# Kernel tuning notes

Hardware: AMD Instinct MI355X
Metric: run time of the kernel (lower is better)

Reference implementation:

```python
import jax, jax.numpy as jnp
import numpy as np

B, S, HIDDEN = 8, 2048, 1024
NUM_GROUPS, NUM_VARS = 2, 320
CODEVECTOR_DIM = 256
TAU = 2.0  # module hardcodes self.temperature = 2
EPS_U = 1e-6


def setup_inputs() -> dict:
    key = jax.random.key(0)
    k1, k2, k3, k4 = jax.random.split(key, 4)
    hidden_states = jax.random.normal(k1, (B, S, HIDDEN), dtype=jnp.float32)
    W = jax.random.normal(k2, (NUM_GROUPS * NUM_VARS, HIDDEN), dtype=jnp.float32) * 0.02
    b = jnp.zeros((NUM_GROUPS * NUM_VARS,), dtype=jnp.float32)
    codevectors = jax.random.normal(
        k3, (1, NUM_GROUPS * NUM_VARS, CODEVECTOR_DIM // NUM_GROUPS), dtype=jnp.float32)
    gumbel_u = jax.random.uniform(
        k4, (B * S * NUM_GROUPS, NUM_VARS), minval=EPS_U, maxval=1.0 - EPS_U, dtype=jnp.float32)
    return {"hidden_states": hidden_states, "W": W, "b": b,
            "codevectors": codevectors, "gumbel_u": gumbel_u}


def reference(hidden_states, W, b, codevectors, gumbel_u):
    Bs, Ss, H = hidden_states.shape
    G, V = NUM_GROUPS, NUM_VARS
    N = Bs * Ss
    # weight_proj: [B,S,H] -> [B,S,G*V]
    logits = jnp.einsum('bsh,vh->bsv', hidden_states, W) + b
    logits = logits.reshape(N * G, V)
    # gumbel_softmax(tau=2, hard=True) -- training path
    gumbel = -jnp.log(-jnp.log(gumbel_u))
    y_soft = jax.nn.softmax((logits + gumbel) / TAU, axis=-1)
    idx = jnp.argmax(y_soft, axis=-1)
    y_hard = jax.nn.one_hot(idx, V, dtype=y_soft.dtype)
    # straight-through (hard value, soft gradient)
    codevector_probs = y_hard + y_soft - jax.lax.stop_gradient(y_soft)
    # perplexity over the soft (non-gumbel) distribution
    soft_dist = jax.nn.softmax(logits.reshape(N, G, V), axis=-1)
    marginal = soft_dist.mean(axis=0)                      # [G, V]
    perplexity = jnp.exp(-jnp.sum(marginal * jnp.log(marginal + 1e-7), axis=-1)).sum()
    # one-hot probs x codevectors, grouped sum: [N,G,V] x [G,V,d] -> [N,G,d]
    cv = codevectors.reshape(G, V, CODEVECTOR_DIM // G)
    out = jnp.einsum('ngv,gvd->ngd', codevector_probs.reshape(N, G, V), cv)
    out = out.reshape(Bs, Ss, CODEVECTOR_DIM)
    return out, perplexity
```

## Files before the change

### kernel.cpp

```cpp
#include <hip/hip_runtime.h>
#include <math.h>

#define NROWS 16384
#define HIDDEN 1024
#define NVARS 320
#define NCOLS 640
#define CVDIM 256
#define OUT_ELEMS (NROWS * CVDIM)

#define BM 64
#define BK 32
#define NTHREADS 512
#define LGS 324
#define BUFS 12288

typedef __attribute__((ext_vector_type(8))) short short8;
typedef __attribute__((ext_vector_type(4))) float floatx4;

__device__ __forceinline__ unsigned f32_to_bf16(float f) {
    unsigned u = __builtin_bit_cast(unsigned, f);
    return (u + 0x7FFFu + ((u >> 16) & 1u)) >> 16;
}
__device__ __forceinline__ float bf16_to_f32(ushort u) {
    return __builtin_bit_cast(float, ((unsigned)u) << 16);
}

__global__ __launch_bounds__(256) void convert_bf16_kernel(
    const float* __restrict__ src, ushort* __restrict__ dst, int n8)
{
    const int i = blockIdx.x * 256 + threadIdx.x;
    if (i >= n8) return;
    const float4* s = reinterpret_cast<const float4*>(src) + (size_t)i * 2;
    const float4 v0 = s[0];
    const float4 v1 = s[1];
    uint4 p;
    p.x = f32_to_bf16(v0.x) | (f32_to_bf16(v0.y) << 16);
    p.y = f32_to_bf16(v0.z) | (f32_to_bf16(v0.w) << 16);
    p.z = f32_to_bf16(v1.x) | (f32_to_bf16(v1.y) << 16);
    p.w = f32_to_bf16(v1.z) | (f32_to_bf16(v1.w) << 16);
    reinterpret_cast<uint4*>(dst)[i] = p;
}

__device__ __forceinline__ void async16(const ushort* g, ushort* l) {
    __builtin_amdgcn_global_load_lds(
        (const __attribute__((address_space(1))) void*)g,
        (__attribute__((address_space(3))) void*)l,
        16, 0, 0);
}

__global__ __launch_bounds__(NTHREADS, 4) void fused_gvq_kernel(
    const float* __restrict__ X,
    const ushort* __restrict__ Wbf,
    const float* __restrict__ bias,
    const float* __restrict__ gu,
    const float* __restrict__ cv,
    float* __restrict__ out,
    float* __restrict__ marginal)
{
    __shared__ __align__(16) ushort lds[2 * BUFS];

    const int tid = threadIdx.x;
    const int lane = tid & 63;
    const int w = tid >> 6;
    const int wm = w >> 2;
    const int wn = w & 3;
    const int mtile = blockIdx.x >> 1;
    const int g = blockIdx.x & 1;
    const int m0 = mtile * BM;
    const int n0 = g * NVARS;

    const int rm = lane & 15;
    const int kc = lane >> 4;

    floatx4 acc[2][5];
#pragma unroll
    for (int i = 0; i < 2; ++i)
#pragma unroll
        for (int j = 0; j < 5; ++j) acc[i][j] = (floatx4){0.f, 0.f, 0.f, 0.f};

    const int arow = tid >> 3;
    const int ak4 = (tid & 7) * 4;
    const float* Abase = X + (size_t)(m0 + arow) * HIDDEN + ak4;

#define WRITE_A(dstAs, v)                                                     \
    {                                                                         \
        uint2 pk;                                                             \
        pk.x = f32_to_bf16((v).x) | (f32_to_bf16((v).y) << 16);               \
        pk.y = f32_to_bf16((v).z) | (f32_to_bf16((v).w) << 16);               \
        *reinterpret_cast<uint2*>(&(dstAs)[arow * 32 + ak4]) = pk;            \
    }

#define ISSUE_B(dstBs, kk)                                                    \
    {                                                                         \
        int c = tid;                                                          \
        async16(Wbf + (size_t)(n0 + (c >> 2)) * HIDDEN + (kk) + (c & 3) * 8,  \
                (dstBs) + c * 8);                                             \
        c = tid + 512;                                                        \
        async16(Wbf + (size_t)(n0 + (c >> 2)) * HIDDEN + (kk) + (c & 3) * 8,  \
                (dstBs) + c * 8);                                             \
        if (tid < 256) {                                                      \
            c = tid + 1024;                                                   \
            async16(Wbf + (size_t)(n0 + (c >> 2)) * HIDDEN + (kk) + (c & 3) * 8, \
                    (dstBs) + c * 8);                                         \
        }                                                                     \
    }

    float4 areg = *reinterpret_cast<const float4*>(Abase);
    WRITE_A(lds, areg);
    ISSUE_B(lds + 2048, 0);
    areg = *reinterpret_cast<const float4*>(Abase + BK);
    __syncthreads();

    for (int t = 0; t < 32; ++t) {
        const int cur = t & 1;
        ushort* base_c = lds + cur * BUFS;
        ushort* base_n = lds + (cur ^ 1) * BUFS;

        if (t < 31) {
            WRITE_A(base_n, areg);
            ISSUE_B(base_n + 2048, (t + 1) * BK);
        }
        if (t < 30)
            areg = *reinterpret_cast<const float4*>(Abase + (t + 2) * BK);

        const short8* Asv = reinterpret_cast<const short8*>(base_c);
        const short8* Bsv = reinterpret_cast<const short8*>(base_c + 2048);
        short8 af[2], bf[5];
#pragma unroll
        for (int i = 0; i < 2; ++i)
            af[i] = Asv[(wm * 32 + i * 16 + rm) * 4 + kc];
#pragma unroll
        for (int j = 0; j < 5; ++j)
            bf[j] = Bsv[(wn * 80 + j * 16 + rm) * 4 + kc];
#pragma unroll
        for (int i = 0; i < 2; ++i)
#pragma unroll
            for (int j = 0; j < 5; ++j)
                acc[i][j] = __builtin_amdgcn_mfma_f32_16x16x32_bf16(
                    af[i], bf[j], acc[i][j], 0, 0, 0);
        __syncthreads();
    }

    const int cl = lane & 15;
    const int r4 = (lane >> 4) * 4;

    {
        float bj[5];
#pragma unroll
        for (int j = 0; j < 5; ++j) bj[j] = bias[n0 + wn * 80 + j * 16 + cl];
#pragma unroll
        for (int i = 0; i < 2; ++i)
#pragma unroll
            for (int j = 0; j < 5; ++j) {
                const int col = wn * 80 + j * 16 + cl;
#pragma unroll
                for (int q = 0; q < 4; ++q) {
                    const int lrow = wm * 32 + i * 16 + r4 + q;
                    lds[lrow * LGS + col] = (ushort)f32_to_bf16(acc[i][j][q] + bj[j]);
                }
            }
    }

    float gup[8][5];
#pragma unroll
    for (int s = 0; s < 8; ++s) {
        const int n = m0 + s * 8 + w;
        const size_t goff = ((size_t)n * 2 + g) * NVARS + lane;
#pragma unroll
        for (int j = 0; j < 5; ++j) gup[s][j] = gu[goff + j * 64];
    }
    __syncthreads();

    float macc[5];
#pragma unroll
    for (int j = 0; j < 5; ++j) macc[j] = 0.f;

#pragma unroll
    for (int s = 0; s < 8; ++s) {
        const int lrow = s * 8 + w;
        const int n = m0 + lrow;

        float lg[5];
#pragma unroll
        for (int j = 0; j < 5; ++j)
            lg[j] = bf16_to_f32(lds[lrow * LGS + lane + j * 64]);

        float bk = lg[0] - __logf(-__logf(gup[s][0]));
        int bi = lane;
#pragma unroll
        for (int j = 1; j < 5; ++j) {
            const float kj = lg[j] - __logf(-__logf(gup[s][j]));
            const int v = lane + j * 64;
            if (kj > bk) { bk = kj; bi = v; }
        }
#pragma unroll
        for (int sh = 32; sh > 0; sh >>= 1) {
            const float ok = __shfl_xor(bk, sh);
            const int oi = __shfl_xor(bi, sh);
            if (ok > bk || (ok == bk && oi < bi)) { bk = ok; bi = oi; }
        }

        float p[5], sume = 0.f;
#pragma unroll
        for (int j = 0; j < 5; ++j) { p[j] = __expf(lg[j]); sume += p[j]; }
#pragma unroll
        for (int sh = 32; sh > 0; sh >>= 1) sume += __shfl_xor(sume, sh);
        const float inv = 1.f / sume;
#pragma unroll
        for (int j = 0; j < 5; ++j) macc[j] += p[j] * inv;

        const float2* cvrow =
            reinterpret_cast<const float2*>(cv + (size_t)(n0 + bi) * 128);
        reinterpret_cast<float2*>(out + (size_t)n * CVDIM + g * 128)[lane] = cvrow[lane];
    }

    __syncthreads();
    float* smr = reinterpret_cast<float*>(lds);
#pragma unroll
    for (int j = 0; j < 5; ++j) smr[w * NVARS + lane + j * 64] = macc[j];
    __syncthreads();
    if (tid < NVARS) {
        float sm = 0.f;
#pragma unroll
        for (int ww = 0; ww < 8; ++ww) sm += smr[ww * NVARS + tid];
        atomicAdd(&marginal[n0 + tid], sm);
    }
}

__global__ void perplexity_kernel(const float* __restrict__ marginal,
                                  float* __restrict__ out)
{
    const int lane = threadIdx.x;
    float h0 = 0.0f, h1 = 0.0f;
    for (int v = lane; v < NVARS; v += 64) {
        const float m0 = marginal[v] * (1.0f / (float)NROWS);
        h0 += m0 * logf(m0 + 1e-7f);
        const float m1 = marginal[NVARS + v] * (1.0f / (float)NROWS);
        h1 += m1 * logf(m1 + 1e-7f);
    }
#pragma unroll
    for (int s = 32; s > 0; s >>= 1) {
        h0 += __shfl_xor(h0, s);
        h1 += __shfl_xor(h1, s);
    }
    if (lane == 0) out[OUT_ELEMS] = expf(-h0) + expf(-h1);
}

extern "C" void kernel_launch(void* const* d_in, const int* in_sizes, int n_in,
                              void* d_out, int out_size, void* d_ws, size_t ws_size,
                              hipStream_t stream) {
    const float* X    = (const float*)d_in[0];
    const float* W    = (const float*)d_in[1];
    const float* bias = (const float*)d_in[2];
    const float* cv   = (const float*)d_in[3];
    const float* gu   = (const float*)d_in[4];
    float* out = (float*)d_out;

    ushort* Wbf      = (ushort*)d_ws;
    float*  marginal = (float*)(Wbf + (size_t)NCOLS * HIDDEN);

    hipMemsetAsync(marginal, 0, NCOLS * sizeof(float), stream);

    convert_bf16_kernel<<<(NCOLS * HIDDEN / 8 + 255) / 256, 256, 0, stream>>>(
        W, Wbf, NCOLS * HIDDEN / 8);

    fused_gvq_kernel<<<(NROWS / BM) * 2, NTHREADS, 0, stream>>>(
        X, Wbf, bias, gu, cv, out, marginal);

    perplexity_kernel<<<1, 64, 0, stream>>>(marginal, out);
}
```

Baseline: 68.72 us.

## Stage A tiles in 128-wide swizzled LDS chunks and remap blocks per XCD

A is now loaded in 128-column chunks, 16 floats per thread, and stored to LDS as bf16 with an XOR swizzle. A is double-buffered separately from the per-32-K B tiles, so fewer A global load and convert phases are interleaved with the MFMA loop. Block indices are remapped so that consecutive M tiles, and both groups of each tile, land on the same XCD, which is meant to improve L2 reuse. LDS use grows from 48KB to 72KB, which may cut occupancy under the 4-blocks launch bound, and there are more registers in flight for A.

```diff
diff --git a/kernel.cpp b/kernel.cpp
--- a/kernel.cpp
+++ b/kernel.cpp
@@ -10,9 +10,15 @@
 
 #define BM 64
 #define BK 32
+#define AK 128
 #define NTHREADS 512
 #define LGS 324
-#define BUFS 12288
+
+#define A0_OFF 0
+#define A1_OFF 8192
+#define B0_OFF 16384
+#define B1_OFF 26624
+#define LDS_USHORTS 36864
 
 typedef __attribute__((ext_vector_type(8))) short short8;
 typedef __attribute__((ext_vector_type(4))) float floatx4;
@@ -57,15 +63,19 @@
     float* __restrict__ out,
     float* __restrict__ marginal)
 {
-    __shared__ __align__(16) ushort lds[2 * BUFS];
+    __shared__ __align__(16) ushort lds[LDS_USHORTS];
+    char* ldsb = reinterpret_cast<char*>(lds);
 
     const int tid = threadIdx.x;
     const int lane = tid & 63;
     const int w = tid >> 6;
     const int wm = w >> 2;
     const int wn = w & 3;
-    const int mtile = blockIdx.x >> 1;
-    const int g = blockIdx.x & 1;
+
+    const int wg = blockIdx.x;
+    const int xcd = wg & 7, slot = wg >> 3;
+    const int mtile = xcd * 32 + (slot >> 1);
+    const int g = slot & 1;
     const int m0 = mtile * BM;
     const int n0 = g * NVARS;
 
@@ -79,66 +89,80 @@
         for (int j = 0; j < 5; ++j) acc[i][j] = (floatx4){0.f, 0.f, 0.f, 0.f};
 
     const int arow = tid >> 3;
-    const int ak4 = (tid & 7) * 4;
-    const float* Abase = X + (size_t)(m0 + arow) * HIDDEN + ak4;
-
-#define WRITE_A(dstAs, v)                                                     \
-    {                                                                         \
-        uint2 pk;                                                             \
-        pk.x = f32_to_bf16((v).x) | (f32_to_bf16((v).y) << 16);               \
-        pk.y = f32_to_bf16((v).z) | (f32_to_bf16((v).w) << 16);               \
-        *reinterpret_cast<uint2*>(&(dstAs)[arow * 32 + ak4]) = pk;            \
-    }
-
-#define ISSUE_B(dstBs, kk)                                                    \
-    {                                                                         \
-        int c = tid;                                                          \
-        async16(Wbf + (size_t)(n0 + (c >> 2)) * HIDDEN + (kk) + (c & 3) * 8,  \
-                (dstBs) + c * 8);                                             \
-        c = tid + 512;                                                        \
-        async16(Wbf + (size_t)(n0 + (c >> 2)) * HIDDEN + (kk) + (c & 3) * 8,  \
-                (dstBs) + c * 8);                                             \
-        if (tid < 256) {                                                      \
-            c = tid + 1024;                                                   \
-            async16(Wbf + (size_t)(n0 + (c >> 2)) * HIDDEN + (kk) + (c & 3) * 8, \
-                    (dstBs) + c * 8);                                         \
-        }                                                                     \
-    }
-
-    float4 areg = *reinterpret_cast<const float4*>(Abase);
-    WRITE_A(lds, areg);
-    ISSUE_B(lds + 2048, 0);
-    areg = *reinterpret_cast<const float4*>(Abase + BK);
-    __syncthreads();
-
-    for (int t = 0; t < 32; ++t) {
-        const int cur = t & 1;
-        ushort* base_c = lds + cur * BUFS;
-        ushort* base_n = lds + (cur ^ 1) * BUFS;
-
-        if (t < 31) {
-            WRITE_A(base_n, areg);
-            ISSUE_B(base_n + 2048, (t + 1) * BK);
+    const int acol = (tid & 7) * 16;
+    const float* Aptr = X + (size_t)(m0 + arow) * HIDDEN + acol;
+    const int arow_b = arow * 256;
+    const int akb0 = (acol * 2) ^ ((arow & 7) << 4);
+    const int akb1 = akb0 ^ 16;
+
+    float4 ar0, ar1, ar2, ar3;
+#define LOAD_A(j) { const float* p = Aptr + (j) * AK;                          \
+    ar0 = *(const float4*)(p);     ar1 = *(const float4*)(p + 4);              \
+    ar2 = *(const float4*)(p + 8); ar3 = *(const float4*)(p + 12); }
+
+#define WRITE_A(aoff) { uint4 lo, hi;                                          \
+    lo.x = f32_to_bf16(ar0.x) | (f32_to_bf16(ar0.y) << 16);                    \
+    lo.y = f32_to_bf16(ar0.z) | (f32_to_bf16(ar0.w) << 16);                    \
+    lo.z = f32_to_bf16(ar1.x) | (f32_to_bf16(ar1.y) << 16);                    \
+    lo.w = f32_to_bf16(ar1.z) | (f32_to_bf16(ar1.w) << 16);                    \
+    hi.x = f32_to_bf16(ar2.x) | (f32_to_bf16(ar2.y) << 16);                    \
+    hi.y = f32_to_bf16(ar2.z) | (f32_to_bf16(ar2.w) << 16);                    \
+    hi.z = f32_to_bf16(ar3.x) | (f32_to_bf16(ar3.y) << 16);                    \
+    hi.w = f32_to_bf16(ar3.z) | (f32_to_bf16(ar3.w) << 16);                    \
+    *(uint4*)(ldsb + (aoff) * 2 + arow_b + akb0) = lo;                         \
+    *(uint4*)(ldsb + (aoff) * 2 + arow_b + akb1) = hi; }
+
+#define ISSUE_B(bboff, kk) {                                                   \
+    int c = tid;                                                               \
+    async16(Wbf + (size_t)(n0 + (c >> 2)) * HIDDEN + (kk) + (c & 3) * 8,       \
+            lds + (bboff) + c * 8);                                            \
+    c = tid + 512;                                                             \
+    async16(Wbf + (size_t)(n0 + (c >> 2)) * HIDDEN + (kk) + (c & 3) * 8,       \
+            lds + (bboff) + c * 8);                                            \
+    if (tid < 256) { c = tid + 1024;                                           \
+    async16(Wbf + (size_t)(n0 + (c >> 2)) * HIDDEN + (kk) + (c & 3) * 8,       \
+            lds + (bboff) + c * 8); } }
+
+    LOAD_A(0); WRITE_A(A0_OFF);
+    LOAD_A(1);
+    ISSUE_B(B0_OFF, 0);
+    __syncthreads();
+
+    const int swzr = (rm & 7) << 4;
+    const int kc16 = kc * 16;
+    const int rowa0_b = (wm * 32 + rm) * 256;
+    const int rowa1_b = (wm * 32 + 16 + rm) * 256;
+    int boff[5];
+#pragma unroll
+    for (int j = 0; j < 5; ++j) boff[j] = (wn * 80 + j * 16 + rm) * 64 + kc16;
+
+    for (int tt = 0; tt < 8; ++tt) {
+        const int abase  = (tt & 1) ? A1_OFF : A0_OFF;
+        const int abasen = (tt & 1) ? A0_OFF : A1_OFF;
+#pragma unroll
+        for (int ph = 0; ph < 4; ++ph) {
+            const int t = tt * 4 + ph;
+            const int bcur  = (t & 1) ? B1_OFF : B0_OFF;
+            const int bnext = (t & 1) ? B0_OFF : B1_OFF;
+            if (t < 31) ISSUE_B(bnext, (t + 1) * BK);
+            if (ph == 1 && tt < 7) WRITE_A(abasen);
+            if (ph == 2 && tt < 6) LOAD_A(tt + 2);
+
+            const int kphys = (ph * 64 + kc16) ^ swzr;
+            short8 af[2], bf[5];
+            af[0] = *(const short8*)(ldsb + abase * 2 + rowa0_b + kphys);
+            af[1] = *(const short8*)(ldsb + abase * 2 + rowa1_b + kphys);
+#pragma unroll
+            for (int j = 0; j < 5; ++j)
+                bf[j] = *(const short8*)(ldsb + bcur * 2 + boff[j]);
+#pragma unroll
+            for (int i = 0; i < 2; ++i)
+#pragma unroll
+                for (int j = 0; j < 5; ++j)
+                    acc[i][j] = __builtin_amdgcn_mfma_f32_16x16x32_bf16(
+                        af[i], bf[j], acc[i][j], 0, 0, 0);
+            __syncthreads();
         }
-        if (t < 30)
-            areg = *reinterpret_cast<const float4*>(Abase + (t + 2) * BK);
-
-        const short8* Asv = reinterpret_cast<const short8*>(base_c);
-        const short8* Bsv = reinterpret_cast<const short8*>(base_c + 2048);
-        short8 af[2], bf[5];
-#pragma unroll
-        for (int i = 0; i < 2; ++i)
-            af[i] = Asv[(wm * 32 + i * 16 + rm) * 4 + kc];
-#pragma unroll
-        for (int j = 0; j < 5; ++j)
-            bf[j] = Bsv[(wn * 80 + j * 16 + rm) * 4 + kc];
-#pragma unroll
-        for (int i = 0; i < 2; ++i)
-#pragma unroll
-            for (int j = 0; j < 5; ++j)
-                acc[i][j] = __builtin_amdgcn_mfma_f32_16x16x32_bf16(
-                    af[i], bf[j], acc[i][j], 0, 0, 0);
-        __syncthreads();
     }
 
     const int cl = lane & 15;
```

Result: no change. 68.15 us (-0.8%).
